# Kernel tuning notes

Hardware: AMD Instinct MI355X
Metric: run time of the kernel (lower is better)

Reference implementation:

```python
import jax, jax.numpy as jnp
import numpy as np

# MPI 15-joint skeleton: 0 head,1 neck,2 rsho,3 relb,4 rwri,5 lsho,6 lelb,7 lwri,
# 8 rhip,9 rknee,10 rankle,11 lhip,12 lknee,13 lankle,14 hip/spine
LEFT_BONES = np.array([[1, 5], [5, 6], [6, 7], [14, 11], [11, 12], [12, 13]], dtype=np.int32)
RIGHT_BONES = np.array([[1, 2], [2, 3], [3, 4], [14, 8], [8, 9], [9, 10]], dtype=np.int32)

FLEN = 512.0   # focal length (pixels)
CX, CY = 512.0, 256.0  # principal point
R_CAM = np.eye(3, dtype=np.float32)  # fixed drone->camera rotation

B, J = 262144, 15


def setup_inputs() -> dict:
    key = jax.random.key(0)
    k1, k2, k3, k4 = jax.random.split(key, 4)
    pose3d = jax.random.normal(k1, (B, 3, J), dtype=jnp.float32)
    pose_2d = jax.random.normal(k2, (B, 2, J), dtype=jnp.float32)
    # near-identity rotations so camera-frame depth stays well away from 0
    R_drone = jnp.eye(3, dtype=jnp.float32)[None] + 0.05 * jax.random.normal(k3, (B, 3, 3), dtype=jnp.float32)
    C_drone = jax.random.normal(k4, (B, 3, 1), dtype=jnp.float32)
    C_drone = C_drone.at[:, 2, :].add(-5.0)  # put camera behind the pose along z
    return {"pose3d": pose3d, "pose_2d": pose_2d, "R_drone": R_drone, "C_drone": C_drone}


def _forward(pose3d, pose_2d, R_drone, C_drone):
    lb = jnp.asarray(LEFT_BONES)
    rb = jnp.asarray(RIGHT_BONES)
    # bone length (squared) for each side: gather endpoints, diff, sum over xyz
    dl = pose3d[:, :, lb[:, 0]] - pose3d[:, :, lb[:, 1]]   # [B,3,6]
    dr = pose3d[:, :, rb[:, 0]] - pose3d[:, :, rb[:, 1]]   # [B,3,6]
    len_l = jnp.sum(dl * dl, axis=1)                        # [B,6]
    len_r = jnp.sum(dr * dr, axis=1)                        # [B,6]
    sym = jnp.mean((len_l - len_r) ** 2)                    # mean over bones and batch

    # take_bone_projection: camera frame = R_cam @ R_drone^T @ (P - C), pinhole projection
    P = jnp.einsum('bji,bjk->bik', R_drone, pose3d - C_drone)          # R_drone^T @ (P - C), [B,3,J]
    P = jnp.einsum('ij,bjk->bik', jnp.asarray(R_CAM), P)               # [B,3,J]
    z = P[:, 2]                                                         # [B,J]
    u = FLEN * P[:, 0] / z + CX
    v = FLEN * P[:, 1] / z + CY
    projected_2d = jnp.stack([u, v], axis=1)                            # [B,2,J]
    proj = jnp.mean((projected_2d - pose_2d) ** 2)
    return jnp.stack([sym, proj])


def reference(pose3d, pose_2d, R_drone, C_drone):
    return _forward(pose3d, pose_2d, R_drone, C_drone)
```

## Files before the change

### kernel.cpp

```cpp
#include <hip/hip_runtime.h>


typedef float f4u __attribute__((ext_vector_type(4), aligned(4)));
typedef float f2u __attribute__((ext_vector_type(2), aligned(4)));

__global__ __launch_bounds__(256) void pose_calib_main(
    const float* __restrict__ pose3d,
    const float* __restrict__ pose2d,
    const float* __restrict__ Rd,
    const float* __restrict__ Cd,
    double* __restrict__ partial,
    int B)
{
    const int p = blockIdx.x * 256 + threadIdx.x;
    double sym_d = 0.0, proj_d = 0.0;

    if (p < B) {
        const float* g3 = pose3d + (size_t)p * 45;
        const float* g2 = pose2d + (size_t)p * 30;
        const float* gR = Rd + (size_t)p * 9;
        const float* gC = Cd + (size_t)p * 3;

        float X[45], pu[15], pv[15], Rr[9], Cc[3];
        #pragma unroll
        for (int k = 0; k < 11; ++k) {
            f4u v = *(const f4u*)(g3 + 4 * k);
            X[4 * k] = v.x; X[4 * k + 1] = v.y; X[4 * k + 2] = v.z; X[4 * k + 3] = v.w;
        }
        X[44] = g3[44];
        #pragma unroll
        for (int k = 0; k < 7; ++k) {
            f4u v = *(const f4u*)(g2 + 4 * k);
            float* d = (k < 4) ? &pu[4 * k] : &pv[4 * k - 15];
            (void)d;
            int base = 4 * k;
            float vals[4] = {v.x, v.y, v.z, v.w};
            #pragma unroll
            for (int t = 0; t < 4; ++t) {
                int idx = base + t;
                if (idx < 15) pu[idx] = vals[t]; else pv[idx - 15] = vals[t];
            }
        }
        { f2u v = *(const f2u*)(g2 + 28); pv[13] = v.x; pv[14] = v.y; }
        { f4u v = *(const f4u*)(gR); Rr[0] = v.x; Rr[1] = v.y; Rr[2] = v.z; Rr[3] = v.w; }
        { f4u v = *(const f4u*)(gR + 4); Rr[4] = v.x; Rr[5] = v.y; Rr[6] = v.z; Rr[7] = v.w; }
        Rr[8] = gR[8];
        { f2u v = *(const f2u*)(gC); Cc[0] = v.x; Cc[1] = v.y; }
        Cc[2] = gC[2];

        const int lb0[6] = {1, 5, 6, 14, 11, 12}, lb1[6] = {5, 6, 7, 11, 12, 13};
        const int rb0[6] = {1, 2, 3, 14, 8, 9},   rb1[6] = {2, 3, 4, 8, 9, 10};
        #pragma unroll
        for (int k = 0; k < 6; ++k) {
            double ll = 0.0, lr = 0.0;
            #pragma unroll
            for (int c = 0; c < 3; ++c) {
                double dl = (double)X[c * 15 + lb0[k]] - (double)X[c * 15 + lb1[k]];
                double dr = (double)X[c * 15 + rb0[k]] - (double)X[c * 15 + rb1[k]];
                ll += dl * dl;
                lr += dr * dr;
            }
            double d = ll - lr;
            sym_d += d * d;
        }

        const double R00 = Rr[0], R01 = Rr[1], R02 = Rr[2];
        const double R10 = Rr[3], R11 = Rr[4], R12 = Rr[5];
        const double R20 = Rr[6], R21 = Rr[7], R22 = Rr[8];
        const double C0 = Cc[0], C1 = Cc[1], C2 = Cc[2];
        #pragma unroll
        for (int j = 0; j < 15; ++j) {
            double q0 = (double)X[j]      - C0;
            double q1 = (double)X[15 + j] - C1;
            double q2 = (double)X[30 + j] - C2;
            double P0 = R00 * q0 + R10 * q1 + R20 * q2;
            double P1 = R01 * q0 + R11 * q1 + R21 * q2;
            double P2 = R02 * q0 + R12 * q1 + R22 * q2;
            double rz = 1.0 / P2;
            double du = 512.0 * P0 * rz + 512.0 - (double)pu[j];
            double dv = 512.0 * P1 * rz + 256.0 - (double)pv[j];
            proj_d += du * du + dv * dv;
        }
    }

    #pragma unroll
    for (int off = 32; off > 0; off >>= 1) {
        sym_d  += __shfl_down(sym_d,  off, 64);
        proj_d += __shfl_down(proj_d, off, 64);
    }
    __shared__ double s_sym[4], s_proj[4];
    const int lane = threadIdx.x & 63;
    const int wid  = threadIdx.x >> 6;
    if (lane == 0) { s_sym[wid] = sym_d; s_proj[wid] = proj_d; }
    __syncthreads();
    if (threadIdx.x == 0) {
        partial[2 * (size_t)blockIdx.x]     = s_sym[0] + s_sym[1] + s_sym[2] + s_sym[3];
        partial[2 * (size_t)blockIdx.x + 1] = s_proj[0] + s_proj[1] + s_proj[2] + s_proj[3];
    }
}

__global__ __launch_bounds__(256) void pose_calib_finish(
    const double* __restrict__ partial, int nblk,
    float* __restrict__ out, double inv_n_sym, double inv_n_proj)
{
    const double2* p2 = (const double2*)partial;
    double ss = 0.0, pp = 0.0;
    for (int i = threadIdx.x; i < nblk; i += 256) {
        double2 v = p2[i];
        ss += v.x;
        pp += v.y;
    }
    #pragma unroll
    for (int off = 32; off > 0; off >>= 1) {
        ss += __shfl_down(ss, off, 64);
        pp += __shfl_down(pp, off, 64);
    }
    __shared__ double s_s[4], s_p[4];
    const int lane = threadIdx.x & 63;
    const int wid  = threadIdx.x >> 6;
    if (lane == 0) { s_s[wid] = ss; s_p[wid] = pp; }
    __syncthreads();
    if (threadIdx.x == 0) {
        double S = s_s[0] + s_s[1] + s_s[2] + s_s[3];
        double P = s_p[0] + s_p[1] + s_p[2] + s_p[3];
        out[0] = (float)(S * inv_n_sym);
        out[1] = (float)(P * inv_n_proj);
    }
}

extern "C" void kernel_launch(void* const* d_in, const int* in_sizes, int n_in,
                              void* d_out, int out_size, void* d_ws, size_t ws_size,
                              hipStream_t stream) {
    const float* pose3d = (const float*)d_in[0];
    const float* pose2d = (const float*)d_in[1];
    const float* Rd     = (const float*)d_in[2];
    const float* Cd     = (const float*)d_in[3];

    const int B = in_sizes[3] / 3;
    const int nblk = (B + 255) / 256;

    double* partial = (double*)d_ws;

    pose_calib_main<<<nblk, 256, 0, stream>>>(pose3d, pose2d, Rd, Cd, partial, B);
    pose_calib_finish<<<1, 256, 0, stream>>>(
        partial, nblk, (float*)d_out,
        1.0 / ((double)B * 6.0), 1.0 / ((double)B * 30.0));
}
```

Baseline: 22.41 us.

## Fuse final reduction into main kernel via last-block atomic counter; fp32 symmetry math

Merges the separate finish kernel into the main kernel. Each block publishes its partial sums with release stores, and the last block to increment an atomic counter does the final reduction. The counter is reset with a memset before launch. The bone-symmetry arithmetic also moves from double to float, which cuts FP64 work at some cost in accuracy. This removes one kernel launch but adds a memset and an atomic per block.

```diff
diff --git a/kernel.cpp b/kernel.cpp
--- a/kernel.cpp
+++ b/kernel.cpp
@@ -4,16 +4,19 @@
 typedef float f4u __attribute__((ext_vector_type(4), aligned(4)));
 typedef float f2u __attribute__((ext_vector_type(2), aligned(4)));
 
-__global__ __launch_bounds__(256) void pose_calib_main(
+__global__ __launch_bounds__(256) void pose_calib_fused(
     const float* __restrict__ pose3d,
     const float* __restrict__ pose2d,
     const float* __restrict__ Rd,
     const float* __restrict__ Cd,
-    double* __restrict__ partial,
-    int B)
+    double* __restrict__ part,
+    unsigned* __restrict__ cnt,
+    float* __restrict__ out,
+    int B, int nblk, double inv_n_sym, double inv_n_proj)
 {
     const int p = blockIdx.x * 256 + threadIdx.x;
-    double sym_d = 0.0, proj_d = 0.0;
+    float  sym_f  = 0.0f;
+    double proj_d = 0.0;
 
     if (p < B) {
         const float* g3 = pose3d + (size_t)p * 45;
@@ -21,108 +24,101 @@
         const float* gR = Rd + (size_t)p * 9;
         const float* gC = Cd + (size_t)p * 3;
 
-        float X[45], pu[15], pv[15], Rr[9], Cc[3];
+        float X[45], P2a[30], Rr[9], Cc[3];
         #pragma unroll
         for (int k = 0; k < 11; ++k) {
             f4u v = *(const f4u*)(g3 + 4 * k);
-            X[4 * k] = v.x; X[4 * k + 1] = v.y; X[4 * k + 2] = v.z; X[4 * k + 3] = v.w;
+            X[4*k] = v.x; X[4*k+1] = v.y; X[4*k+2] = v.z; X[4*k+3] = v.w;
         }
         X[44] = g3[44];
         #pragma unroll
         for (int k = 0; k < 7; ++k) {
             f4u v = *(const f4u*)(g2 + 4 * k);
-            float* d = (k < 4) ? &pu[4 * k] : &pv[4 * k - 15];
-            (void)d;
-            int base = 4 * k;
-            float vals[4] = {v.x, v.y, v.z, v.w};
-            #pragma unroll
-            for (int t = 0; t < 4; ++t) {
-                int idx = base + t;
-                if (idx < 15) pu[idx] = vals[t]; else pv[idx - 15] = vals[t];
-            }
+            P2a[4*k] = v.x; P2a[4*k+1] = v.y; P2a[4*k+2] = v.z; P2a[4*k+3] = v.w;
         }
-        { f2u v = *(const f2u*)(g2 + 28); pv[13] = v.x; pv[14] = v.y; }
-        { f4u v = *(const f4u*)(gR); Rr[0] = v.x; Rr[1] = v.y; Rr[2] = v.z; Rr[3] = v.w; }
-        { f4u v = *(const f4u*)(gR + 4); Rr[4] = v.x; Rr[5] = v.y; Rr[6] = v.z; Rr[7] = v.w; }
+        { f2u v = *(const f2u*)(g2 + 28); P2a[28] = v.x; P2a[29] = v.y; }
+        { f4u v = *(const f4u*)(gR);     Rr[0]=v.x; Rr[1]=v.y; Rr[2]=v.z; Rr[3]=v.w; }
+        { f4u v = *(const f4u*)(gR + 4); Rr[4]=v.x; Rr[5]=v.y; Rr[6]=v.z; Rr[7]=v.w; }
         Rr[8] = gR[8];
         { f2u v = *(const f2u*)(gC); Cc[0] = v.x; Cc[1] = v.y; }
         Cc[2] = gC[2];
 
-        const int lb0[6] = {1, 5, 6, 14, 11, 12}, lb1[6] = {5, 6, 7, 11, 12, 13};
-        const int rb0[6] = {1, 2, 3, 14, 8, 9},   rb1[6] = {2, 3, 4, 8, 9, 10};
+        const int lb0[6] = {1,5,6,14,11,12}, lb1[6] = {5,6,7,11,12,13};
+        const int rb0[6] = {1,2,3,14,8,9},   rb1[6] = {2,3,4,8,9,10};
         #pragma unroll
         for (int k = 0; k < 6; ++k) {
-            double ll = 0.0, lr = 0.0;
+            float ll = 0.f, lr = 0.f;
             #pragma unroll
             for (int c = 0; c < 3; ++c) {
-                double dl = (double)X[c * 15 + lb0[k]] - (double)X[c * 15 + lb1[k]];
-                double dr = (double)X[c * 15 + rb0[k]] - (double)X[c * 15 + rb1[k]];
+                float dl = X[c*15 + lb0[k]] - X[c*15 + lb1[k]];
+                float dr = X[c*15 + rb0[k]] - X[c*15 + rb1[k]];
                 ll += dl * dl;
                 lr += dr * dr;
             }
-            double d = ll - lr;
-            sym_d += d * d;
+            float d = ll - lr;
+            sym_f += d * d;
         }
 
-        const double R00 = Rr[0], R01 = Rr[1], R02 = Rr[2];
-        const double R10 = Rr[3], R11 = Rr[4], R12 = Rr[5];
-        const double R20 = Rr[6], R21 = Rr[7], R22 = Rr[8];
-        const double C0 = Cc[0], C1 = Cc[1], C2 = Cc[2];
         #pragma unroll
         for (int j = 0; j < 15; ++j) {
-            double q0 = (double)X[j]      - C0;
-            double q1 = (double)X[15 + j] - C1;
-            double q2 = (double)X[30 + j] - C2;
-            double P0 = R00 * q0 + R10 * q1 + R20 * q2;
-            double P1 = R01 * q0 + R11 * q1 + R21 * q2;
-            double P2 = R02 * q0 + R12 * q1 + R22 * q2;
-            double rz = 1.0 / P2;
-            double du = 512.0 * P0 * rz + 512.0 - (double)pu[j];
-            double dv = 512.0 * P1 * rz + 256.0 - (double)pv[j];
+            double q0 = (double)X[j]      - (double)Cc[0];
+            double q1 = (double)X[15 + j] - (double)Cc[1];
+            double q2 = (double)X[30 + j] - (double)Cc[2];
+            double P0 = (double)Rr[0]*q0 + (double)Rr[3]*q1 + (double)Rr[6]*q2;
+            double P1 = (double)Rr[1]*q0 + (double)Rr[4]*q1 + (double)Rr[7]*q2;
+            double Pz = (double)Rr[2]*q0 + (double)Rr[5]*q1 + (double)Rr[8]*q2;
+            double rz = 1.0 / Pz;
+            double du = 512.0 * P0 * rz + 512.0 - (double)P2a[j];
+            double dv = 512.0 * P1 * rz + 256.0 - (double)P2a[15 + j];
             proj_d += du * du + dv * dv;
         }
     }
 
+    double sym_d = (double)sym_f;
     #pragma unroll
     for (int off = 32; off > 0; off >>= 1) {
         sym_d  += __shfl_down(sym_d,  off, 64);
         proj_d += __shfl_down(proj_d, off, 64);
     }
     __shared__ double s_sym[4], s_proj[4];
+    __shared__ int amLast;
     const int lane = threadIdx.x & 63;
     const int wid  = threadIdx.x >> 6;
     if (lane == 0) { s_sym[wid] = sym_d; s_proj[wid] = proj_d; }
     __syncthreads();
+
     if (threadIdx.x == 0) {
-        partial[2 * (size_t)blockIdx.x]     = s_sym[0] + s_sym[1] + s_sym[2] + s_sym[3];
-        partial[2 * (size_t)blockIdx.x + 1] = s_proj[0] + s_proj[1] + s_proj[2] + s_proj[3];
+        double sd = s_sym[0] + s_sym[1] + s_sym[2] + s_sym[3];
+        double pd = s_proj[0] + s_proj[1] + s_proj[2] + s_proj[3];
+        __hip_atomic_store(&part[2*(size_t)blockIdx.x],     sd,
+                           __ATOMIC_RELEASE, __HIP_MEMORY_SCOPE_AGENT);
+        __hip_atomic_store(&part[2*(size_t)blockIdx.x + 1], pd,
+                           __ATOMIC_RELEASE, __HIP_MEMORY_SCOPE_AGENT);
+        unsigned old = __hip_atomic_fetch_add(cnt, 1u,
+                           __ATOMIC_ACQ_REL, __HIP_MEMORY_SCOPE_AGENT);
+        amLast = (old == (unsigned)nblk - 1);
     }
-}
+    __syncthreads();
+    if (!amLast) return;
 
-__global__ __launch_bounds__(256) void pose_calib_finish(
-    const double* __restrict__ partial, int nblk,
-    float* __restrict__ out, double inv_n_sym, double inv_n_proj)
-{
-    const double2* p2 = (const double2*)partial;
     double ss = 0.0, pp = 0.0;
     for (int i = threadIdx.x; i < nblk; i += 256) {
-        double2 v = p2[i];
-        ss += v.x;
-        pp += v.y;
+        ss += __hip_atomic_load(&part[2*(size_t)i],
+                                __ATOMIC_RELAXED, __HIP_MEMORY_SCOPE_AGENT);
+        pp += __hip_atomic_load(&part[2*(size_t)i + 1],
+                                __ATOMIC_RELAXED, __HIP_MEMORY_SCOPE_AGENT);
     }
     #pragma unroll
     for (int off = 32; off > 0; off >>= 1) {
         ss += __shfl_down(ss, off, 64);
         pp += __shfl_down(pp, off, 64);
     }
-    __shared__ double s_s[4], s_p[4];
-    const int lane = threadIdx.x & 63;
-    const int wid  = threadIdx.x >> 6;
-    if (lane == 0) { s_s[wid] = ss; s_p[wid] = pp; }
+    __syncthreads();
+    if (lane == 0) { s_sym[wid] = ss; s_proj[wid] = pp; }
     __syncthreads();
     if (threadIdx.x == 0) {
-        double S = s_s[0] + s_s[1] + s_s[2] + s_s[3];
-        double P = s_p[0] + s_p[1] + s_p[2] + s_p[3];
+        double S = s_sym[0] + s_sym[1] + s_sym[2] + s_sym[3];
+        double P = s_proj[0] + s_proj[1] + s_proj[2] + s_proj[3];
         out[0] = (float)(S * inv_n_sym);
         out[1] = (float)(P * inv_n_proj);
     }
@@ -136,13 +132,15 @@
     const float* Rd     = (const float*)d_in[2];
     const float* Cd     = (const float*)d_in[3];
 
-    const int B = in_sizes[3] / 3;
+    const int B    = in_sizes[3] / 3;
     const int nblk = (B + 255) / 256;
 
-    double* partial = (double*)d_ws;
+    double*   part = (double*)d_ws;
+    unsigned* cnt  = (unsigned*)((char*)d_ws + (size_t)nblk * 2 * sizeof(double));
 
-    pose_calib_main<<<nblk, 256, 0, stream>>>(pose3d, pose2d, Rd, Cd, partial, B);
-    pose_calib_finish<<<1, 256, 0, stream>>>(
-        partial, nblk, (float*)d_out,
-        1.0 / ((double)B * 6.0), 1.0 / ((double)B * 30.0));
+    hipMemsetAsync(cnt, 0, sizeof(unsigned), stream);
+
+    pose_calib_fused<<<nblk, 256, 0, stream>>>(
+        pose3d, pose2d, Rd, Cd, part, cnt, (float*)d_out,
+        B, nblk, 1.0 / ((double)B * 6.0), 1.0 / ((double)B * 30.0));
 }
```

Result: slower. 86.35 us (+285.3%).

## Stage per-pose data in LDS via direct global-to-LDS loads and split joints across waves

Applied to the files above, without the earlier changes.

Each block now covers 64 poses. The four waves cooperatively copy the contiguous slab of pose3d, pose_2d, R and C into shared memory using global_load_lds 16-byte transfers, which gives fully coalesced loads in place of per-thread strided loads. Every wave then handles a subset of the joints and bones for the same 64 poses, so per-thread register pressure and work drop, while the block count grows fourfold. The finish kernel is widened to 1024 threads to absorb the larger partial array. The costs are an added barrier, more LDS traffic, and a partial-slab fallback path that uses scalar loads.

```diff
diff --git a/kernel.cpp b/kernel.cpp
--- a/kernel.cpp
+++ b/kernel.cpp
@@ -1,8 +1,43 @@
 #include <hip/hip_runtime.h>
 
 
-typedef float f4u __attribute__((ext_vector_type(4), aligned(4)));
-typedef float f2u __attribute__((ext_vector_type(2), aligned(4)));
+typedef const __attribute__((address_space(1))) void* gas1_t;
+typedef __attribute__((address_space(3))) void* las3_t;
+
+__device__ __forceinline__ void gl16(const float* g, float* l) {
+    __builtin_amdgcn_global_load_lds((gas1_t)g, (las3_t)l, 16, 0, 0);
+}
+
+__device__ __forceinline__ void proj_joint(
+    const float* __restrict__ X, const float* __restrict__ P2, int j,
+    const double (&Rr)[9], double C0, double C1, double C2, double& proj_d)
+{
+    double q0 = (double)X[j]      - C0;
+    double q1 = (double)X[15 + j] - C1;
+    double q2 = (double)X[30 + j] - C2;
+    double P0 = Rr[0] * q0 + Rr[3] * q1 + Rr[6] * q2;
+    double P1 = Rr[1] * q0 + Rr[4] * q1 + Rr[7] * q2;
+    double Pz = Rr[2] * q0 + Rr[5] * q1 + Rr[8] * q2;
+    double rz = 1.0 / Pz;
+    double du = 512.0 * P0 * rz + 512.0 - (double)P2[j];
+    double dv = 512.0 * P1 * rz + 256.0 - (double)P2[15 + j];
+    proj_d += du * du + dv * dv;
+}
+
+__device__ __forceinline__ void bone_term(
+    const float* __restrict__ X, int l0, int l1, int r0, int r1, double& sym_d)
+{
+    double ll = 0.0, lr = 0.0;
+    #pragma unroll
+    for (int c = 0; c < 3; ++c) {
+        double dl = (double)X[c * 15 + l0] - (double)X[c * 15 + l1];
+        double dr = (double)X[c * 15 + r0] - (double)X[c * 15 + r1];
+        ll += dl * dl;
+        lr += dr * dr;
+    }
+    double d = ll - lr;
+    sym_d += d * d;
+}
 
 __global__ __launch_bounds__(256) void pose_calib_main(
     const float* __restrict__ pose3d,
@@ -12,75 +47,123 @@
     double* __restrict__ partial,
     int B)
 {
-    const int p = blockIdx.x * 256 + threadIdx.x;
+    __shared__ float sl[5568];
+    __shared__ double s_sym[4], s_proj[4];
+
+    const int tid  = threadIdx.x;
+    const int lane = tid & 63;
+    const int wid  = tid >> 6;
+    const long long p0 = (long long)blockIdx.x * 64;
+    const bool fullslab = (p0 + 64 <= (long long)B);
+
     double sym_d = 0.0, proj_d = 0.0;
 
-    if (p < B) {
-        const float* g3 = pose3d + (size_t)p * 45;
-        const float* g2 = pose2d + (size_t)p * 30;
-        const float* gR = Rd + (size_t)p * 9;
-        const float* gC = Cd + (size_t)p * 3;
-
-        float X[45], pu[15], pv[15], Rr[9], Cc[3];
+    if (fullslab) {
+        const float* g3 = pose3d + p0 * 45;
+        const float* g2 = pose2d + p0 * 30;
+        const float* gR = Rd + p0 * 9;
+        const float* gC = Cd + p0 * 3;
+
+        if (wid == 0) {
+            #pragma unroll
+            for (int k = 0; k < 6; ++k) gl16(g3 + k * 256 + lane * 4, sl + k * 256);
+        } else if (wid == 1) {
+            #pragma unroll
+            for (int k = 6; k < 11; ++k) gl16(g3 + k * 256 + lane * 4, sl + k * 256);
+            gl16(g3 + 2624 + lane * 4, sl + 2624);
+        } else if (wid == 2) {
+            #pragma unroll
+            for (int k = 0; k < 6; ++k) gl16(g2 + k * 256 + lane * 4, sl + 2880 + k * 256);
+        } else {
+            gl16(g2 + 1536 + lane * 4, sl + 2880 + 1536);
+            gl16(g2 + 1664 + lane * 4, sl + 2880 + 1664);
+            gl16(gR + lane * 4,        sl + 4800);
+            gl16(gR + 256 + lane * 4,  sl + 5056);
+            gl16(gR + 320 + lane * 4,  sl + 5120);
+            if (lane < 48) gl16(gC + lane * 4, sl + 5376);
+        }
+        __syncthreads();
+
+        const float* X  = sl + lane * 45;
+        const float* P2 = sl + 2880 + lane * 30;
+        const float* Rf = sl + 4800 + lane * 9;
+        const float* Cf = sl + 5376 + lane * 3;
+
+        double Rr[9];
         #pragma unroll
-        for (int k = 0; k < 11; ++k) {
-            f4u v = *(const f4u*)(g3 + 4 * k);
-            X[4 * k] = v.x; X[4 * k + 1] = v.y; X[4 * k + 2] = v.z; X[4 * k + 3] = v.w;
+        for (int k = 0; k < 9; ++k) Rr[k] = (double)Rf[k];
+        const double C0 = (double)Cf[0], C1 = (double)Cf[1], C2 = (double)Cf[2];
+
+        if (wid == 0) {
+            proj_joint(X, P2, 0, Rr, C0, C1, C2, proj_d);
+            proj_joint(X, P2, 1, Rr, C0, C1, C2, proj_d);
+            proj_joint(X, P2, 2, Rr, C0, C1, C2, proj_d);
+            proj_joint(X, P2, 3, Rr, C0, C1, C2, proj_d);
+            bone_term(X, 1, 5, 1, 2, sym_d);
+            bone_term(X, 5, 6, 2, 3, sym_d);
+        } else if (wid == 1) {
+            proj_joint(X, P2, 4, Rr, C0, C1, C2, proj_d);
+            proj_joint(X, P2, 5, Rr, C0, C1, C2, proj_d);
+            proj_joint(X, P2, 6, Rr, C0, C1, C2, proj_d);
+            proj_joint(X, P2, 7, Rr, C0, C1, C2, proj_d);
+            bone_term(X, 6, 7, 3, 4, sym_d);
+            bone_term(X, 14, 11, 14, 8, sym_d);
+        } else if (wid == 2) {
+            proj_joint(X, P2, 8, Rr, C0, C1, C2, proj_d);
+            proj_joint(X, P2, 9, Rr, C0, C1, C2, proj_d);
+            proj_joint(X, P2, 10, Rr, C0, C1, C2, proj_d);
+            proj_joint(X, P2, 11, Rr, C0, C1, C2, proj_d);
+            bone_term(X, 11, 12, 8, 9, sym_d);
+        } else {
+            proj_joint(X, P2, 12, Rr, C0, C1, C2, proj_d);
+            proj_joint(X, P2, 13, Rr, C0, C1, C2, proj_d);
+            proj_joint(X, P2, 14, Rr, C0, C1, C2, proj_d);
+            bone_term(X, 12, 13, 9, 10, sym_d);
         }
-        X[44] = g3[44];
-        #pragma unroll
-        for (int k = 0; k < 7; ++k) {
-            f4u v = *(const f4u*)(g2 + 4 * k);
-            float* d = (k < 4) ? &pu[4 * k] : &pv[4 * k - 15];
-            (void)d;
-            int base = 4 * k;
-            float vals[4] = {v.x, v.y, v.z, v.w};
-            #pragma unroll
-            for (int t = 0; t < 4; ++t) {
-                int idx = base + t;
-                if (idx < 15) pu[idx] = vals[t]; else pv[idx - 15] = vals[t];
+    } else {
+        const long long p = p0 + lane;
+        if (p < (long long)B) {
+            const float* g3 = pose3d + p * 45;
+            const float* g2 = pose2d + p * 30;
+            const float* gR = Rd + p * 9;
+            const float* gC = Cd + p * 3;
+            float X[45], P2l[30];
+            #pragma unroll
+            for (int i = 0; i < 45; ++i) X[i] = g3[i];
+            #pragma unroll
+            for (int i = 0; i < 30; ++i) P2l[i] = g2[i];
+            double Rr[9];
+            #pragma unroll
+            for (int k = 0; k < 9; ++k) Rr[k] = (double)gR[k];
+            const double C0 = gC[0], C1 = gC[1], C2 = gC[2];
+            if (wid == 0) {
+                proj_joint(X, P2l, 0, Rr, C0, C1, C2, proj_d);
+                proj_joint(X, P2l, 1, Rr, C0, C1, C2, proj_d);
+                proj_joint(X, P2l, 2, Rr, C0, C1, C2, proj_d);
+                proj_joint(X, P2l, 3, Rr, C0, C1, C2, proj_d);
+                bone_term(X, 1, 5, 1, 2, sym_d);
+                bone_term(X, 5, 6, 2, 3, sym_d);
+            } else if (wid == 1) {
+                proj_joint(X, P2l, 4, Rr, C0, C1, C2, proj_d);
+                proj_joint(X, P2l, 5, Rr, C0, C1, C2, proj_d);
+                proj_joint(X, P2l, 6, Rr, C0, C1, C2, proj_d);
+                proj_joint(X, P2l, 7, Rr, C0, C1, C2, proj_d);
+                bone_term(X, 6, 7, 3, 4, sym_d);
+                bone_term(X, 14, 11, 14, 8, sym_d);
+            } else if (wid == 2) {
+                proj_joint(X, P2l, 8, Rr, C0, C1, C2, proj_d);
+                proj_joint(X, P2l, 9, Rr, C0, C1, C2, proj_d);
+                proj_joint(X, P2l, 10, Rr, C0, C1, C2, proj_d);
+                proj_joint(X, P2l, 11, Rr, C0, C1, C2, proj_d);
+                bone_term(X, 11, 12, 8, 9, sym_d);
+            } else {
+                proj_joint(X, P2l, 12, Rr, C0, C1, C2, proj_d);
+                proj_joint(X, P2l, 13, Rr, C0, C1, C2, proj_d);
+                proj_joint(X, P2l, 14, Rr, C0, C1, C2, proj_d);
+                bone_term(X, 12, 13, 9, 10, sym_d);
             }
         }
-        { f2u v = *(const f2u*)(g2 + 28); pv[13] = v.x; pv[14] = v.y; }
-        { f4u v = *(const f4u*)(gR); Rr[0] = v.x; Rr[1] = v.y; Rr[2] = v.z; Rr[3] = v.w; }
-        { f4u v = *(const f4u*)(gR + 4); Rr[4] = v.x; Rr[5] = v.y; Rr[6] = v.z; Rr[7] = v.w; }
-        Rr[8] = gR[8];
-        { f2u v = *(const f2u*)(gC); Cc[0] = v.x; Cc[1] = v.y; }
-        Cc[2] = gC[2];
-
-        const int lb0[6] = {1, 5, 6, 14, 11, 12}, lb1[6] = {5, 6, 7, 11, 12, 13};
-        const int rb0[6] = {1, 2, 3, 14, 8, 9},   rb1[6] = {2, 3, 4, 8, 9, 10};
-        #pragma unroll
-        for (int k = 0; k < 6; ++k) {
-            double ll = 0.0, lr = 0.0;
-            #pragma unroll
-            for (int c = 0; c < 3; ++c) {
-                double dl = (double)X[c * 15 + lb0[k]] - (double)X[c * 15 + lb1[k]];
-                double dr = (double)X[c * 15 + rb0[k]] - (double)X[c * 15 + rb1[k]];
-                ll += dl * dl;
-                lr += dr * dr;
-            }
-            double d = ll - lr;
-            sym_d += d * d;
-        }
-
-        const double R00 = Rr[0], R01 = Rr[1], R02 = Rr[2];
-        const double R10 = Rr[3], R11 = Rr[4], R12 = Rr[5];
-        const double R20 = Rr[6], R21 = Rr[7], R22 = Rr[8];
-        const double C0 = Cc[0], C1 = Cc[1], C2 = Cc[2];
-        #pragma unroll
-        for (int j = 0; j < 15; ++j) {
-            double q0 = (double)X[j]      - C0;
-            double q1 = (double)X[15 + j] - C1;
-            double q2 = (double)X[30 + j] - C2;
-            double P0 = R00 * q0 + R10 * q1 + R20 * q2;
-            double P1 = R01 * q0 + R11 * q1 + R21 * q2;
-            double P2 = R02 * q0 + R12 * q1 + R22 * q2;
-            double rz = 1.0 / P2;
-            double du = 512.0 * P0 * rz + 512.0 - (double)pu[j];
-            double dv = 512.0 * P1 * rz + 256.0 - (double)pv[j];
-            proj_d += du * du + dv * dv;
-        }
+        __syncthreads();
     }
 
     #pragma unroll
@@ -88,24 +171,21 @@
         sym_d  += __shfl_down(sym_d,  off, 64);
         proj_d += __shfl_down(proj_d, off, 64);
     }
-    __shared__ double s_sym[4], s_proj[4];
-    const int lane = threadIdx.x & 63;
-    const int wid  = threadIdx.x >> 6;
     if (lane == 0) { s_sym[wid] = sym_d; s_proj[wid] = proj_d; }
     __syncthreads();
-    if (threadIdx.x == 0) {
+    if (tid == 0) {
         partial[2 * (size_t)blockIdx.x]     = s_sym[0] + s_sym[1] + s_sym[2] + s_sym[3];
         partial[2 * (size_t)blockIdx.x + 1] = s_proj[0] + s_proj[1] + s_proj[2] + s_proj[3];
     }
 }
 
-__global__ __launch_bounds__(256) void pose_calib_finish(
+__global__ __launch_bounds__(1024) void pose_calib_finish(
     const double* __restrict__ partial, int nblk,
     float* __restrict__ out, double inv_n_sym, double inv_n_proj)
 {
     const double2* p2 = (const double2*)partial;
     double ss = 0.0, pp = 0.0;
-    for (int i = threadIdx.x; i < nblk; i += 256) {
+    for (int i = threadIdx.x; i < nblk; i += 1024) {
         double2 v = p2[i];
         ss += v.x;
         pp += v.y;
@@ -115,14 +195,15 @@
         ss += __shfl_down(ss, off, 64);
         pp += __shfl_down(pp, off, 64);
     }
-    __shared__ double s_s[4], s_p[4];
+    __shared__ double s_s[16], s_p[16];
     const int lane = threadIdx.x & 63;
     const int wid  = threadIdx.x >> 6;
     if (lane == 0) { s_s[wid] = ss; s_p[wid] = pp; }
     __syncthreads();
     if (threadIdx.x == 0) {
-        double S = s_s[0] + s_s[1] + s_s[2] + s_s[3];
-        double P = s_p[0] + s_p[1] + s_p[2] + s_p[3];
+        double S = 0.0, P = 0.0;
+        #pragma unroll
+        for (int k = 0; k < 16; ++k) { S += s_s[k]; P += s_p[k]; }
         out[0] = (float)(S * inv_n_sym);
         out[1] = (float)(P * inv_n_proj);
     }
@@ -136,13 +217,13 @@
     const float* Rd     = (const float*)d_in[2];
     const float* Cd     = (const float*)d_in[3];
 
-    const int B = in_sizes[3] / 3;
-    const int nblk = (B + 255) / 256;
+    const int B    = in_sizes[3] / 3;
+    const int nblk = (B + 63) / 64;
 
     double* partial = (double*)d_ws;
 
     pose_calib_main<<<nblk, 256, 0, stream>>>(pose3d, pose2d, Rd, Cd, partial, B);
-    pose_calib_finish<<<1, 256, 0, stream>>>(
+    pose_calib_finish<<<1, 1024, 0, stream>>>(
         partial, nblk, (float*)d_out,
         1.0 / ((double)B * 6.0), 1.0 / ((double)B * 30.0));
 }
```

Result: slower. 23.91 us (+6.7%).
